# Kernel tuning notes

Measured on AMD Instinct MI355X. Metric: run time of the kernel, lower is better.

## Reference

```python
import jax, jax.numpy as jnp
import numpy as np

EPS = 1e-5
B, C_IN, C_OUT, N, K = 2, 8, 128, 65536, 16


def setup_inputs() -> dict:
    key = jax.random.key(0)
    ks = jax.random.split(key, 20)
    f = lambda k, shape, s=0.05: jax.random.normal(k, shape, dtype=jnp.float32) * s
    pv = lambda k, shape: jax.random.uniform(k, shape, dtype=jnp.float32) + 0.5
    return {
        "x": jax.random.normal(ks[0], (B, C_IN, N), dtype=jnp.float32),
        "neighbors": jax.random.randint(ks[1], (B, K, N), 0, N, dtype=jnp.int32),
        # BatchNorm1d (eval mode)
        "g1": pv(ks[2], (C_IN,)), "b1": f(ks[3], (C_IN,)),
        "m1": f(ks[4], (C_IN,)), "v1": pv(ks[5], (C_IN,)),
        # conv1: 1x1 Conv1d C_in -> C_out, with bias
        "w1": f(ks[6], (C_OUT, C_IN)), "c1b": f(ks[7], (C_OUT,)),
        # conv2[0]: BatchNorm2d(C_in)
        "g2": pv(ks[8], (C_IN,)), "b2": f(ks[9], (C_IN,)),
        "m2": f(ks[10], (C_IN,)), "v2": pv(ks[11], (C_IN,)),
        # conv2[1]: 1x1 Conv2d C_in -> C_out, no bias
        "wA": f(ks[12], (C_OUT, C_IN)),
        # conv2[2]: BatchNorm2d(C_out)
        "g3": pv(ks[13], (C_OUT,)), "b3": f(ks[14], (C_OUT,)),
        "m3": f(ks[15], (C_OUT,)), "v3": pv(ks[16], (C_OUT,)),
        # conv2[4]: 1x1 Conv2d C_out -> C_out, no bias
        "wB": f(ks[17], (C_OUT, C_OUT)),
        # final: 1x1 Conv1d 2*C_out -> C_out, with bias
        "wf": f(ks[18], (C_OUT, 2 * C_OUT)), "bf": f(ks[19], (C_OUT,)),
    }


def reference(x, neighbors, g1, b1, m1, v1, w1, c1b, g2, b2, m2, v2, wA,
              g3, b3, m3, v3, wB, wf, bf):
    # BatchNorm1d (eval): y = x*scale + shift, per channel
    s1 = g1 * jax.lax.rsqrt(v1 + EPS)
    xn = x * s1[None, :, None] + (b1 - m1 * s1)[None, :, None]  # (B, C_in, N)

    # per-point embedding: 1x1 conv
    point_emb = jnp.einsum('oc,bcn->bon', w1, xn) + c1b[None, :, None]  # (B, C_out, N)

    # gather neighbors 1..K-1 along point dim, subtract center point
    idx = neighbors[:, 1:, :]  # (B, K-1, N)
    gathered = jnp.take_along_axis(xn[:, :, None, :], idx[:, None, :, :], axis=3)  # (B, C_in, K-1, N)
    neigh = gathered - xn[:, :, None, :]

    # conv2: BN2d -> 1x1 conv -> BN2d -> ReLU -> 1x1 conv
    s2 = g2 * jax.lax.rsqrt(v2 + EPS)
    h = neigh * s2[None, :, None, None] + (b2 - m2 * s2)[None, :, None, None]
    h = jnp.einsum('oc,bckn->bokn', wA, h)  # (B, C_out, K-1, N)
    s3 = g3 * jax.lax.rsqrt(v3 + EPS)
    h = h * s3[None, :, None, None] + (b3 - m3 * s3)[None, :, None, None]
    h = jax.nn.relu(h)
    h = jnp.einsum('oc,bckn->bokn', wB, h)
    neigh_emb = jnp.max(h, axis=2)  # max over neighbors -> (B, C_out, N)

    cat = jnp.concatenate((point_emb, neigh_emb), axis=1)  # (B, 2*C_out, N)
    return jnp.einsum('oc,bcn->bon', wf, cat) + bf[None, :, None]
```

## Files before the change

kernel.cpp:

```cpp
#include <hip/hip_runtime.h>
#include <hip/hip_bf16.h>

typedef unsigned short u16;
typedef unsigned int u32;
typedef short bf16x8 __attribute__((ext_vector_type(8)));
typedef float f32x4 __attribute__((ext_vector_type(4)));

#define EPSV 1e-5f
#define WS_A3L   0
#define WS_WB    8192
#define WS_WCAT  40960
#define WS_XH    81920

union U4 { uint4 q; bf16x8 v; };

__device__ __forceinline__ u16 f2bf(float f) {
    union { __hip_bfloat16 h; u16 u; } cv;
    cv.h = __float2bfloat16(f);
    return cv.u;
}
__device__ __forceinline__ u32 pack_rne(float a, float b) {
    u32 ua = __float_as_uint(a), ub = __float_as_uint(b);
    ua = ua + 0x7FFFu + ((ua >> 16) & 1u);
    ub = ub + 0x7FFFu + ((ub >> 16) & 1u);
    return (ua >> 16) | (ub & 0xFFFF0000u);
}

__global__ __launch_bounds__(256) void prep_kernel(
    const float* g1, const float* b1, const float* m1, const float* v1,
    const float* w1, const float* c1b,
    const float* g2, const float* b2, const float* m2, const float* v2,
    const float* wA,
    const float* g3, const float* b3, const float* m3, const float* v3,
    const float* wB, const float* wf, const float* bfv,
    u16* A3L, u16* wBh, u16* Wc)
{
    __shared__ float wfL[16384];
    __shared__ float w1s[1024];
    __shared__ float c1s[128];
    __shared__ float s1[8], be1[8], s2[8], be2[8];
    __shared__ float w1fS[128][8];
    __shared__ float cbS[128];
    int t = threadIdx.x;

    for (int i = t; i < 16384; i += 256) wfL[i] = wf[((i >> 7) << 8) + (i & 127)];
    for (int i = t; i < 1024; i += 256) w1s[i] = w1[i];
    if (t < 128) c1s[t] = c1b[t];
    if (t < 8) {
        float s = g1[t] * rsqrtf(v1[t] + EPSV); s1[t] = s; be1[t] = b1[t] - m1[t] * s;
        float u = g2[t] * rsqrtf(v2[t] + EPSV); s2[t] = u; be2[t] = b2[t] - m2[t] * u;
    }
    __syncthreads();

    {
        int o = t >> 1, half = t & 1;
        float a0 = 0.f, a1 = 0.f, a2 = 0.f, a3 = 0.f, cb = 0.f;
        const float* wro = wfL + o * 128;
        int i0 = half * 4;
        for (int c = 0; c < 128; c++) {
            float f = wro[c];
            const float* wr = w1s + c * 8 + i0;
            a0 += f * wr[0]; a1 += f * wr[1]; a2 += f * wr[2]; a3 += f * wr[3];
            if (half) cb += f * c1s[c];
        }
        w1fS[o][i0] = a0; w1fS[o][i0 + 1] = a1; w1fS[o][i0 + 2] = a2; w1fS[o][i0 + 3] = a3;
        if (half) cbS[o] = cb;
    }
    __syncthreads();

    if (t < 128) {
        int o = t;
        float s3 = g3[o] * rsqrtf(v3[o] + EPSV);
        float be3 = b3[o] - m3[o] * s3;
        float csum = 0.f;
        #pragma unroll
        for (int i = 0; i < 8; i++) {
            float wv = wA[o * 8 + i];
            A3L[o * 32 + i] = f2bf(s3 * wv * s2[i] * s1[i]);
            csum += wv * be2[i];
        }
        A3L[o * 32 + 8] = f2bf(s3 * csum + be3);
        for (int k = 9; k < 32; k++) A3L[o * 32 + k] = 0;

        float bs = bfv[o] + cbS[o];
        #pragma unroll
        for (int i = 0; i < 8; i++) {
            float w1f = w1fS[o][i];
            bs += w1f * be1[i];
            Wc[o * 160 + 128 + i] = f2bf(w1f * s1[i]);
        }
        Wc[o * 160 + 136] = f2bf(bs);
        for (int k = 137; k < 160; k++) Wc[o * 160 + k] = 0;
    }
    for (int j = t; j < 16384; j += 256) {
        int o = j >> 7, c = j & 127;
        Wc[o * 160 + c] = f2bf(wf[o * 256 + 128 + c]);
    }
    {
        u32* wbo = (u32*)wBh;
        for (int j = t; j < 8192; j += 256)
            wbo[j] = pack_rne(wB[2 * j], wB[2 * j + 1]);
    }
}

__global__ __launch_bounds__(256) void xhat_kernel(const float* __restrict__ x,
                                                   float* __restrict__ xh)
{
    int t = blockIdx.x * 256 + threadIdx.x;
    int b = t >> 16, n = t & 65535;
    float4 a, c;
    a.x = x[(((b << 3) + 0) << 16) | n];
    a.y = x[(((b << 3) + 1) << 16) | n];
    a.z = x[(((b << 3) + 2) << 16) | n];
    a.w = x[(((b << 3) + 3) << 16) | n];
    c.x = x[(((b << 3) + 4) << 16) | n];
    c.y = x[(((b << 3) + 5) << 16) | n];
    c.z = x[(((b << 3) + 6) << 16) | n];
    c.w = x[(((b << 3) + 7) << 16) | n];
    float4* o = (float4*)xh + ((size_t)t << 1);
    o[0] = a; o[1] = c;
}

#define S1(P, BUF)                                                            \
    {                                                                         \
        U4 bfr;                                                               \
        if (quad == 0)      bfr.q = DXs[((P) << 4) + l15];                    \
        else if (quad == 1) bfr.q = make_uint4(0x00003F80u, 0u, 0u, 0u);      \
        else                bfr.q = make_uint4(0u, 0u, 0u, 0u);               \
        f32x4 z0 = {0.f, 0.f, 0.f, 0.f}, z1 = {0.f, 0.f, 0.f, 0.f};           \
        z0 = __builtin_amdgcn_mfma_f32_16x16x32_bf16(a3f[0], bfr.v, z0, 0, 0, 0); \
        z1 = __builtin_amdgcn_mfma_f32_16x16x32_bf16(a3f[1], bfr.v, z1, 0, 0, 0); \
        u32 w00, w01, w10, w11;                                               \
        asm("v_cvt_pk_bf16_f32 %0, %1, %2" : "=v"(w00)                        \
            : "v"(fmaxf(z0[0], 0.f)), "v"(fmaxf(z0[1], 0.f)));                \
        asm("v_cvt_pk_bf16_f32 %0, %1, %2" : "=v"(w01)                        \
            : "v"(fmaxf(z0[2], 0.f)), "v"(fmaxf(z0[3], 0.f)));                \
        asm("v_cvt_pk_bf16_f32 %0, %1, %2" : "=v"(w10)                        \
            : "v"(fmaxf(z1[0], 0.f)), "v"(fmaxf(z1[1], 0.f)));                \
        asm("v_cvt_pk_bf16_f32 %0, %1, %2" : "=v"(w11)                        \
            : "v"(fmaxf(z1[2], 0.f)), "v"(fmaxf(z1[3], 0.f)));                \
        u32* ab = (u32*)Abuf + (BUF) * 1024 + (l15 << 6) + ((quad & 1) << 1); \
        int gA = ((w << 2) + (quad >> 1)) ^ (l15 & 7);                        \
        int gB = ((w << 2) + 2 + (quad >> 1)) ^ (l15 & 7);                    \
        *(uint2*)(ab + (gA << 2)) = make_uint2(w00, w01);                     \
        *(uint2*)(ab + (gB << 2)) = make_uint2(w10, w11);                     \
    }

#define S2(P, BUF)                                                            \
    {                                                                         \
        f32x4 acc0 = {0.f, 0.f, 0.f, 0.f}, acc1 = {0.f, 0.f, 0.f, 0.f};       \
        _Pragma("unroll")                                                     \
        for (int kt = 0; kt < 4; ++kt) {                                      \
            U4 a; a.q = Abuf[BUF][l15][((kt << 2) + quad) ^ (l15 & 7)];       \
            acc0 = __builtin_amdgcn_mfma_f32_16x16x32_bf16(a.v, wBf[0][kt], acc0, 0, 0, 0); \
            acc1 = __builtin_amdgcn_mfma_f32_16x16x32_bf16(a.v, wBf[1][kt], acc1, 0, 0, 0); \
        }                                                                     \
        float m0 = fmaxf(fmaxf(fmaxf(acc0[0], acc0[1]), acc0[2]), acc0[3]);   \
        float m1 = fmaxf(fmaxf(fmaxf(acc1[0], acc1[1]), acc1[2]), acc1[3]);   \
        m0 = fmaxf(m0, __shfl_xor(m0, 16, 64));                               \
        m0 = fmaxf(m0, __shfl_xor(m0, 32, 64));                               \
        m1 = fmaxf(m1, __shfl_xor(m1, 16, 64));                               \
        m1 = fmaxf(m1, __shfl_xor(m1, 32, 64));                               \
        if (l < 32)                                                           \
            NEu16[(P) * 168 + (w << 5) + l] =                                 \
                (u16)((__float_as_uint((quad == 0) ? m0 : m1) + 0x8000u) >> 16); \
    }

__global__ __launch_bounds__(256, 6) void heavy_kernel(
    const float* __restrict__ xh, const int* __restrict__ nbr,
    const u16* __restrict__ A3Lg, const u16* __restrict__ wBh,
    const u16* __restrict__ Wcat, float* __restrict__ out)
{
    __shared__ uint4 DXs[256];
    __shared__ uint4 Abuf[2][16][16];
    __shared__ uint4 NExq[16 * 21];
    u16* NEu16 = (u16*)NExq;
    int t = threadIdx.x;
    int w = t >> 6, l = t & 63;
    int quad = l >> 4, l15 = l & 15;

    bf16x8 wBf[2][4];
    #pragma unroll
    for (int j = 0; j < 2; j++)
        #pragma unroll
        for (int kt = 0; kt < 4; kt++) {
            U4 u; u.q = *(const uint4*)(wBh + (w * 32 + j * 16 + l15) * 128 + kt * 32 + quad * 8);
            wBf[j][kt] = u.v;
        }
    bf16x8 a3f[2];
    #pragma unroll
    for (int mi = 0; mi < 2; mi++) {
        U4 u; u.q = *(const uint4*)(A3Lg + (((2 * w + mi) * 16 + l15) << 5) + quad * 8);
        a3f[mi] = u.v;
    }

    int pbase = blockIdx.x << 4;
    int b = pbase >> 16;
    int n0 = pbase & 65535;
    const float4* xq = (const float4*)xh + ((size_t)b << 17);

    for (int j = t; j < 336; j += 256) NExq[j] = make_uint4(0u, 0u, 0u, 0u);

    {
        int pt = t >> 4, slot = t & 15;
        int srow = (slot < 15) ? slot + 1 : 1;
        int idx = nbr[(b << 20) | (srow << 16) | (n0 + pt)];
        float4 ga = xq[(u32)(idx << 1)], gb = xq[(u32)((idx << 1) + 1)];
        float4 ca = xq[(u32)((n0 + pt) << 1)], cb = xq[(u32)(((n0 + pt) << 1) + 1)];
        uint4 d;
        d.x = pack_rne(ga.x - ca.x, ga.y - ca.y);
        d.y = pack_rne(ga.z - ca.z, ga.w - ca.w);
        d.z = pack_rne(gb.x - cb.x, gb.y - cb.y);
        d.w = pack_rne(gb.z - cb.z, gb.w - cb.w);
        DXs[t] = d;
    }
    __syncthreads();

    S1(0, 0)
    __syncthreads();

    for (int p = 0; p < 16; p += 2) {
        S1(p + 1, 1)
        S2(p, 0)
        __syncthreads();
        if (p < 14) S1(p + 2, 0)
        S2(p + 1, 1)
        __syncthreads();
    }

    if (t < 16) {
        const float4* xr = xq + ((u32)(n0 + t) << 1);
        float4 xa = xr[0], xb = xr[1];
        u32* dst = (u32*)NExq + t * 84 + 64;
        dst[0] = pack_rne(xa.x, xa.y);
        dst[1] = pack_rne(xa.z, xa.w);
        dst[2] = pack_rne(xb.x, xb.y);
        dst[3] = pack_rne(xb.z, xb.w);
        dst[4] = 0x3F80u;
    }
    __syncthreads();

    bf16x8 Wcf[2][5];
    #pragma unroll
    for (int mt = 0; mt < 2; mt++)
        #pragma unroll
        for (int kt = 0; kt < 5; kt++) {
            U4 u; u.q = *(const uint4*)(Wcat + (w * 32 + mt * 16 + l15) * 160 + kt * 32 + quad * 8);
            Wcf[mt][kt] = u.v;
        }
    f32x4 oa[2];
    oa[0] = (f32x4){0.f, 0.f, 0.f, 0.f};
    oa[1] = (f32x4){0.f, 0.f, 0.f, 0.f};
    #pragma unroll
    for (int kt = 0; kt < 5; ++kt) {
        U4 u; u.q = NExq[l15 * 21 + kt * 4 + quad];
        oa[0] = __builtin_amdgcn_mfma_f32_16x16x32_bf16(Wcf[0][kt], u.v, oa[0], 0, 0, 0);
        oa[1] = __builtin_amdgcn_mfma_f32_16x16x32_bf16(Wcf[1][kt], u.v, oa[1], 0, 0, 0);
    }
    #pragma unroll
    for (int mt = 0; mt < 2; ++mt) {
        int ob = w * 32 + mt * 16 + quad * 4;
        #pragma unroll
        for (int r = 0; r < 4; ++r)
            out[(((b << 7) + ob + r) << 16) + n0 + l15] = oa[mt][r];
    }
}

extern "C" void kernel_launch(void* const* d_in, const int* in_sizes, int n_in,
                              void* d_out, int out_size, void* d_ws, size_t ws_size,
                              hipStream_t stream) {
    const float* x   = (const float*)d_in[0];
    const int*   nbr = (const int*)d_in[1];
    const float* g1  = (const float*)d_in[2];
    const float* b1  = (const float*)d_in[3];
    const float* m1  = (const float*)d_in[4];
    const float* v1  = (const float*)d_in[5];
    const float* w1  = (const float*)d_in[6];
    const float* c1b = (const float*)d_in[7];
    const float* g2  = (const float*)d_in[8];
    const float* b2  = (const float*)d_in[9];
    const float* m2  = (const float*)d_in[10];
    const float* v2  = (const float*)d_in[11];
    const float* wA  = (const float*)d_in[12];
    const float* g3  = (const float*)d_in[13];
    const float* b3  = (const float*)d_in[14];
    const float* m3  = (const float*)d_in[15];
    const float* v3  = (const float*)d_in[16];
    const float* wB  = (const float*)d_in[17];
    const float* wf  = (const float*)d_in[18];
    const float* bfv = (const float*)d_in[19];

    u16*   A3L  = (u16*)((char*)d_ws + WS_A3L);
    u16*   wBh  = (u16*)((char*)d_ws + WS_WB);
    u16*   Wcat = (u16*)((char*)d_ws + WS_WCAT);
    float* xh   = (float*)((char*)d_ws + WS_XH);
    float* out  = (float*)d_out;

    prep_kernel<<<1, 256, 0, stream>>>(g1, b1, m1, v1, w1, c1b, g2, b2, m2, v2,
                                       wA, g3, b3, m3, v3, wB, wf, bfv, A3L, wBh, Wcat);
    xhat_kernel<<<512, 256, 0, stream>>>(x, xh);
    heavy_kernel<<<8192, 256, 0, stream>>>(xh, nbr, A3L, wBh, Wcat, out);
}
```

Baseline: 243.4 us.

## Switch heavy kernel to 32x32x16 MFMA and merge setup kernels

The neighbor MLP stages now use 32x32x16 bf16 MFMA tiles that cover two points (32 rows) per step, replacing pairs of 16x16x32 MFMAs. That halves the pipeline iterations and barriers and changes how the LDS A-buffer is laid out. The prep and transpose kernels are merged into one multi-block setup kernel so weight conversion runs in parallel across blocks, removing a launch and the large shared staging of wf. The cost is larger register tiles (16-float accumulators) and twice the LDS A-buffer, which may lower occupancy.

```diff
diff --git a/kernel.cpp b/kernel.cpp
--- a/kernel.cpp
+++ b/kernel.cpp
@@ -5,6 +5,7 @@
 typedef unsigned int u32;
 typedef short bf16x8 __attribute__((ext_vector_type(8)));
 typedef float f32x4 __attribute__((ext_vector_type(4)));
+typedef float f32x16 __attribute__((ext_vector_type(16)));
 
 #define EPSV 1e-5f
 #define WS_A3L   0
@@ -26,24 +27,50 @@
     return (ua >> 16) | (ub & 0xFFFF0000u);
 }
 
-__global__ __launch_bounds__(256) void prep_kernel(
+__global__ __launch_bounds__(256) void setup_kernel(
+    const float* __restrict__ x,
     const float* g1, const float* b1, const float* m1, const float* v1,
     const float* w1, const float* c1b,
     const float* g2, const float* b2, const float* m2, const float* v2,
     const float* wA,
     const float* g3, const float* b3, const float* m3, const float* v3,
     const float* wB, const float* wf, const float* bfv,
-    u16* A3L, u16* wBh, u16* Wc)
+    float* __restrict__ xh, u16* A3L, u16* wBh, u16* Wc)
 {
-    __shared__ float wfL[16384];
     __shared__ float w1s[1024];
     __shared__ float c1s[128];
     __shared__ float s1[8], be1[8], s2[8], be2[8];
     __shared__ float w1fS[128][8];
     __shared__ float cbS[128];
-    int t = threadIdx.x;
-
-    for (int i = t; i < 16384; i += 256) wfL[i] = wf[((i >> 7) << 8) + (i & 127)];
+    int bid = blockIdx.x, t = threadIdx.x;
+
+    if (bid < 512) {
+        int tg = (bid << 8) + t;
+        int b = tg >> 16, n = tg & 65535;
+        float4 a, c;
+        a.x = x[(((b << 3) + 0) << 16) | n];
+        a.y = x[(((b << 3) + 1) << 16) | n];
+        a.z = x[(((b << 3) + 2) << 16) | n];
+        a.w = x[(((b << 3) + 3) << 16) | n];
+        c.x = x[(((b << 3) + 4) << 16) | n];
+        c.y = x[(((b << 3) + 5) << 16) | n];
+        c.z = x[(((b << 3) + 6) << 16) | n];
+        c.w = x[(((b << 3) + 7) << 16) | n];
+        float4* o = (float4*)xh + ((size_t)tg << 1);
+        o[0] = a; o[1] = c;
+        return;
+    }
+    int rb = bid - 512;
+    for (int j = (rb << 8) + t; j < 16384; j += 8192) {
+        int o = j >> 7, c = j & 127;
+        Wc[o * 160 + c] = f2bf(wf[o * 256 + 128 + c]);
+    }
+    {
+        int j = (rb << 8) + t;
+        ((u32*)wBh)[j] = pack_rne(wB[2 * j], wB[2 * j + 1]);
+    }
+    if (rb) return;
+
     for (int i = t; i < 1024; i += 256) w1s[i] = w1[i];
     if (t < 128) c1s[t] = c1b[t];
     if (t < 8) {
@@ -55,7 +82,7 @@
     {
         int o = t >> 1, half = t & 1;
         float a0 = 0.f, a1 = 0.f, a2 = 0.f, a3 = 0.f, cb = 0.f;
-        const float* wro = wfL + o * 128;
+        const float* wro = wf + o * 256;
         int i0 = half * 4;
         for (int c = 0; c < 128; c++) {
             float f = wro[c];
@@ -92,78 +119,45 @@
         Wc[o * 160 + 136] = f2bf(bs);
         for (int k = 137; k < 160; k++) Wc[o * 160 + k] = 0;
     }
-    for (int j = t; j < 16384; j += 256) {
-        int o = j >> 7, c = j & 127;
-        Wc[o * 160 + c] = f2bf(wf[o * 256 + 128 + c]);
-    }
-    {
-        u32* wbo = (u32*)wBh;
-        for (int j = t; j < 8192; j += 256)
-            wbo[j] = pack_rne(wB[2 * j], wB[2 * j + 1]);
-    }
-}
-
-__global__ __launch_bounds__(256) void xhat_kernel(const float* __restrict__ x,
-                                                   float* __restrict__ xh)
-{
-    int t = blockIdx.x * 256 + threadIdx.x;
-    int b = t >> 16, n = t & 65535;
-    float4 a, c;
-    a.x = x[(((b << 3) + 0) << 16) | n];
-    a.y = x[(((b << 3) + 1) << 16) | n];
-    a.z = x[(((b << 3) + 2) << 16) | n];
-    a.w = x[(((b << 3) + 3) << 16) | n];
-    c.x = x[(((b << 3) + 4) << 16) | n];
-    c.y = x[(((b << 3) + 5) << 16) | n];
-    c.z = x[(((b << 3) + 6) << 16) | n];
-    c.w = x[(((b << 3) + 7) << 16) | n];
-    float4* o = (float4*)xh + ((size_t)t << 1);
-    o[0] = a; o[1] = c;
 }
 
 #define S1(P, BUF)                                                            \
     {                                                                         \
         U4 bfr;                                                               \
-        if (quad == 0)      bfr.q = DXs[((P) << 4) + l15];                    \
-        else if (quad == 1) bfr.q = make_uint4(0x00003F80u, 0u, 0u, 0u);      \
-        else                bfr.q = make_uint4(0u, 0u, 0u, 0u);               \
-        f32x4 z0 = {0.f, 0.f, 0.f, 0.f}, z1 = {0.f, 0.f, 0.f, 0.f};           \
-        z0 = __builtin_amdgcn_mfma_f32_16x16x32_bf16(a3f[0], bfr.v, z0, 0, 0, 0); \
-        z1 = __builtin_amdgcn_mfma_f32_16x16x32_bf16(a3f[1], bfr.v, z1, 0, 0, 0); \
-        u32 w00, w01, w10, w11;                                               \
-        asm("v_cvt_pk_bf16_f32 %0, %1, %2" : "=v"(w00)                        \
-            : "v"(fmaxf(z0[0], 0.f)), "v"(fmaxf(z0[1], 0.f)));                \
-        asm("v_cvt_pk_bf16_f32 %0, %1, %2" : "=v"(w01)                        \
-            : "v"(fmaxf(z0[2], 0.f)), "v"(fmaxf(z0[3], 0.f)));                \
-        asm("v_cvt_pk_bf16_f32 %0, %1, %2" : "=v"(w10)                        \
-            : "v"(fmaxf(z1[0], 0.f)), "v"(fmaxf(z1[1], 0.f)));                \
-        asm("v_cvt_pk_bf16_f32 %0, %1, %2" : "=v"(w11)                        \
-            : "v"(fmaxf(z1[2], 0.f)), "v"(fmaxf(z1[3], 0.f)));                \
-        u32* ab = (u32*)Abuf + (BUF) * 1024 + (l15 << 6) + ((quad & 1) << 1); \
-        int gA = ((w << 2) + (quad >> 1)) ^ (l15 & 7);                        \
-        int gB = ((w << 2) + 2 + (quad >> 1)) ^ (l15 & 7);                    \
-        *(uint2*)(ab + (gA << 2)) = make_uint2(w00, w01);                     \
-        *(uint2*)(ab + (gB << 2)) = make_uint2(w10, w11);                     \
+        if (hi == 0) bfr.q = DXs[((P) << 5) + l31];                           \
+        else         bfr.q = make_uint4(0x00003F80u, 0u, 0u, 0u);             \
+        f32x16 z = {};                                                        \
+        z = __builtin_amdgcn_mfma_f32_32x32x16_bf16(a3f, bfr.v, z, 0, 0, 0);  \
+        u32* ab = (u32*)Abuf + (BUF) * 2048 + (l31 << 6) + (hi << 1);         \
+        _Pragma("unroll")                                                     \
+        for (int gi = 0; gi < 4; gi++) {                                      \
+            u32 plo, phi;                                                     \
+            asm("v_cvt_pk_bf16_f32 %0, %1, %2" : "=v"(plo)                    \
+                : "v"(fmaxf(z[4 * gi + 0], 0.f)), "v"(fmaxf(z[4 * gi + 1], 0.f))); \
+            asm("v_cvt_pk_bf16_f32 %0, %1, %2" : "=v"(phi)                    \
+                : "v"(fmaxf(z[4 * gi + 2], 0.f)), "v"(fmaxf(z[4 * gi + 3], 0.f))); \
+            int gsw = (((w << 2) + gi) ^ (l31 & 7)) << 2;                     \
+            *(uint2*)(ab + gsw) = make_uint2(plo, phi);                       \
+        }                                                                     \
     }
 
 #define S2(P, BUF)                                                            \
     {                                                                         \
-        f32x4 acc0 = {0.f, 0.f, 0.f, 0.f}, acc1 = {0.f, 0.f, 0.f, 0.f};       \
+        f32x16 acc = {};                                                      \
         _Pragma("unroll")                                                     \
-        for (int kt = 0; kt < 4; ++kt) {                                      \
-            U4 a; a.q = Abuf[BUF][l15][((kt << 2) + quad) ^ (l15 & 7)];       \
-            acc0 = __builtin_amdgcn_mfma_f32_16x16x32_bf16(a.v, wBf[0][kt], acc0, 0, 0, 0); \
-            acc1 = __builtin_amdgcn_mfma_f32_16x16x32_bf16(a.v, wBf[1][kt], acc1, 0, 0, 0); \
+        for (int kt = 0; kt < 8; ++kt) {                                      \
+            U4 a; a.q = Abuf[BUF][l31][((kt << 1) + hi) ^ (l31 & 7)];         \
+            acc = __builtin_amdgcn_mfma_f32_32x32x16_bf16(a.v, wBf[kt], acc, 0, 0, 0); \
         }                                                                     \
-        float m0 = fmaxf(fmaxf(fmaxf(acc0[0], acc0[1]), acc0[2]), acc0[3]);   \
-        float m1 = fmaxf(fmaxf(fmaxf(acc1[0], acc1[1]), acc1[2]), acc1[3]);   \
-        m0 = fmaxf(m0, __shfl_xor(m0, 16, 64));                               \
-        m0 = fmaxf(m0, __shfl_xor(m0, 32, 64));                               \
-        m1 = fmaxf(m1, __shfl_xor(m1, 16, 64));                               \
-        m1 = fmaxf(m1, __shfl_xor(m1, 32, 64));                               \
-        if (l < 32)                                                           \
-            NEu16[(P) * 168 + (w << 5) + l] =                                 \
-                (u16)((__float_as_uint((quad == 0) ? m0 : m1) + 0x8000u) >> 16); \
+        float me = fmaxf(fmaxf(fmaxf(acc[0], acc[1]), fmaxf(acc[2], acc[3])), \
+                         fmaxf(fmaxf(acc[4], acc[5]), fmaxf(acc[6], acc[7]))); \
+        float mo = fmaxf(fmaxf(fmaxf(acc[8], acc[9]), fmaxf(acc[10], acc[11])), \
+                         fmaxf(fmaxf(acc[12], acc[13]), fmaxf(acc[14], acc[15]))); \
+        me = fmaxf(me, __shfl_xor(me, 32, 64));                               \
+        mo = fmaxf(mo, __shfl_xor(mo, 32, 64));                               \
+        float mv = hi ? mo : me;                                              \
+        NEu16[(((P) << 1) + hi) * 168 + (w << 5) + l31] =                     \
+            (u16)((__float_as_uint(mv) + 0x8000u) >> 16);                     \
     }
 
 __global__ __launch_bounds__(256, 6) void heavy_kernel(
@@ -172,26 +166,24 @@
     const u16* __restrict__ Wcat, float* __restrict__ out)
 {
     __shared__ uint4 DXs[256];
-    __shared__ uint4 Abuf[2][16][16];
+    __shared__ uint4 Abuf[2][32][16];
     __shared__ uint4 NExq[16 * 21];
     u16* NEu16 = (u16*)NExq;
     int t = threadIdx.x;
     int w = t >> 6, l = t & 63;
+    int l31 = l & 31, hi = l >> 5;
     int quad = l >> 4, l15 = l & 15;
 
-    bf16x8 wBf[2][4];
-    #pragma unroll
-    for (int j = 0; j < 2; j++)
-        #pragma unroll
-        for (int kt = 0; kt < 4; kt++) {
-            U4 u; u.q = *(const uint4*)(wBh + (w * 32 + j * 16 + l15) * 128 + kt * 32 + quad * 8);
-            wBf[j][kt] = u.v;
-        }
-    bf16x8 a3f[2];
-    #pragma unroll
-    for (int mi = 0; mi < 2; mi++) {
-        U4 u; u.q = *(const uint4*)(A3Lg + (((2 * w + mi) * 16 + l15) << 5) + quad * 8);
-        a3f[mi] = u.v;
+    bf16x8 wBf[8];
+    #pragma unroll
+    for (int kt = 0; kt < 8; kt++) {
+        U4 u; u.q = *(const uint4*)(wBh + (w * 32 + l31) * 128 + kt * 16 + hi * 8);
+        wBf[kt] = u.v;
+    }
+    bf16x8 a3f;
+    {
+        U4 u; u.q = *(const uint4*)(A3Lg + ((w * 32 + l31) << 5) + hi * 8);
+        a3f = u.v;
     }
 
     int pbase = blockIdx.x << 4;
@@ -218,13 +210,9 @@
 
     S1(0, 0)
     __syncthreads();
-
-    for (int p = 0; p < 16; p += 2) {
-        S1(p + 1, 1)
-        S2(p, 0)
-        __syncthreads();
-        if (p < 14) S1(p + 2, 0)
-        S2(p + 1, 1)
+    for (int p = 0; p < 8; ++p) {
+        if (p < 7) S1(p + 1, (p + 1) & 1)
+        S2(p, p & 1)
         __syncthreads();
     }
 
@@ -296,8 +284,8 @@
     float* xh   = (float*)((char*)d_ws + WS_XH);
     float* out  = (float*)d_out;
 
-    prep_kernel<<<1, 256, 0, stream>>>(g1, b1, m1, v1, w1, c1b, g2, b2, m2, v2,
-                                       wA, g3, b3, m3, v3, wB, wf, bfv, A3L, wBh, Wcat);
-    xhat_kernel<<<512, 256, 0, stream>>>(x, xh);
+    setup_kernel<<<544, 256, 0, stream>>>(x, g1, b1, m1, v1, w1, c1b,
+                                          g2, b2, m2, v2, wA, g3, b3, m3, v3,
+                                          wB, wf, bfv, xh, A3L, wBh, Wcat);
     heavy_kernel<<<8192, 256, 0, stream>>>(xh, nbr, A3L, wBh, Wcat, out);
 }
```

Result: faster. 221.1 us (-9.1%).
